# Optimization experiments

Measured on AMD Instinct MI355X. Metric: run time of the kernel, lower is better.

## Reference

```python
import jax, jax.numpy as jnp
import numpy as np

TOP_K = 2
EPS = 1e-6

def setup_inputs() -> dict:
    key = jax.random.key(0)
    ks = jax.random.split(key, 4)
    B, L, D, E, ED = 2, 2048, 2048, 8, 2048
    scale_gu = (6.0 / D) ** 0.5   # kaiming_uniform-ish bound
    scale_dn = (6.0 / ED) ** 0.5
    return {
        "x": jax.random.normal(ks[0], (B, L, D), jnp.float32),
        "router_scale": jnp.ones((D,), jnp.float32),
        "gate_w": jax.random.normal(ks[1], (D, E), jnp.float32) * (D ** -0.5),
        "gate_up": jax.random.uniform(ks[2], (E, D, 2 * ED), jnp.float32, -scale_gu, scale_gu),
        "down": jax.random.uniform(ks[3], (E, ED, D), jnp.float32, -scale_dn, scale_dn),
        "per_expert_scale": jnp.ones((E,), jnp.float32),
    }

def reference(x, router_scale, gate_w, gate_up, down, per_expert_scale):
    B, L, D = x.shape
    E = gate_up.shape[0]
    # --- Router: RMSNorm (no scale) * D^-0.5 * router_scale -> linear -> softmax -> topk -> renorm
    h = x * jax.lax.rsqrt(jnp.mean(x * x, axis=-1, keepdims=True) + EPS)
    h = h * (D ** -0.5) * router_scale
    logits = (h @ gate_w).astype(jnp.float32)            # [B,L,E]
    probs = jax.nn.softmax(logits, axis=-1)
    w, idx = jax.lax.top_k(probs, TOP_K)                 # [B,L,K]
    w = w / jnp.clip(jnp.sum(w, axis=-1, keepdims=True), 1e-12)
    w = w.astype(x.dtype)
    # --- Experts: dense compute over all experts, weighted combine by routing
    N = B * L
    xf = x.reshape(N, D)
    idxf = idx.reshape(N, TOP_K)
    wf = w.reshape(N, TOP_K)
    # combine[n,e] = sum_k wf[n,k] * (idxf[n,k]==e); top_k indices are distinct per token
    combine = jnp.zeros((N, E), x.dtype).at[jnp.arange(N)[:, None], idxf].add(wf)
    hh = jnp.einsum('nd,edf->nef', xf, gate_up)          # [N,E,2*ED]
    gate, up = jnp.split(hh, 2, axis=-1)
    act = jax.nn.gelu(gate, approximate=False) * up      # [N,E,ED]
    y = jnp.einsum('nef,efd->ned', act, down)            # [N,E,D]
    out = jnp.einsum('ne,ned->nd', combine * per_expert_scale, y)
    return out.reshape(B, L, D)
```

## Files before the change

### kernel.cpp

```cpp
#include <hip/hip_runtime.h>
#include <hip/hip_bf16.h>
#include <math.h>

#define NTOK 4096
#define DM   2048
#define NE   8
#define NKT  32

using f32x4  = float __attribute__((ext_vector_type(4)));
using bf16x8 = __bf16 __attribute__((ext_vector_type(8)));
using u32x4  = unsigned int __attribute__((ext_vector_type(4)));

#define SBAR()  __builtin_amdgcn_s_barrier()
#define SCHED() __builtin_amdgcn_sched_barrier(0)

__device__ __forceinline__ unsigned short bf16bits(float f){
  unsigned u = __builtin_bit_cast(unsigned, f);
  return (unsigned short)((u + 0x7fffu + ((u >> 16) & 1u)) >> 16);
}

__device__ __forceinline__ void load_lds16(const void* g, void* l){
  __builtin_amdgcn_global_load_lds(
      (const __attribute__((address_space(1))) unsigned int*)g,
      (__attribute__((address_space(3))) unsigned int*)l, 16, 0, 0);
}

__device__ __forceinline__ unsigned lds_addr(const void* p){
  return (unsigned)(unsigned long long)
      (__attribute__((address_space(3))) const char*)p;
}

template<int IMM>
__device__ __forceinline__ bf16x8 lds_read16(unsigned addr){
  u32x4 r;
  asm volatile("ds_read_b128 %0, %1 offset:%c2" : "=v"(r) : "v"(addr), "i"(IMM));
  return __builtin_bit_cast(bf16x8, r);
}

__global__ __launch_bounds__(256) void router_kernel(
    const float* __restrict__ x, const float* __restrict__ rs,
    const float* __restrict__ gw, const float* __restrict__ pes,
    unsigned short* __restrict__ xbf, int* __restrict__ cnt,
    int* __restrict__ toklist, float* __restrict__ slotw)
{
  const int wv = threadIdx.x >> 6, l = threadIdx.x & 63;
  const int n = blockIdx.x * 4 + wv;
  const float* xr = x + (size_t)n * DM;
  unsigned short* xb = xbf + (size_t)n * DM;
  float ssq = 0.f;
  float lg[8] = {0,0,0,0,0,0,0,0};
  #pragma unroll
  for (int q = 0; q < 8; ++q){
    int c4 = l + 64 * q;
    float4 v = ((const float4*)xr)[c4];
    float4 r = ((const float4*)rs)[c4];
    ssq += v.x*v.x + v.y*v.y + v.z*v.z + v.w*v.w;
    ushort4 o; o.x = bf16bits(v.x); o.y = bf16bits(v.y); o.z = bf16bits(v.z); o.w = bf16bits(v.w);
    ((ushort4*)xb)[c4] = o;
    float xs0 = v.x*r.x, xs1 = v.y*r.y, xs2 = v.z*r.z, xs3 = v.w*r.w;
    const float4* gp = (const float4*)(gw + (size_t)c4 * 32);
    float4 ga, gb;
    ga = gp[0]; gb = gp[1];
    lg[0]+=xs0*ga.x; lg[1]+=xs0*ga.y; lg[2]+=xs0*ga.z; lg[3]+=xs0*ga.w;
    lg[4]+=xs0*gb.x; lg[5]+=xs0*gb.y; lg[6]+=xs0*gb.z; lg[7]+=xs0*gb.w;
    ga = gp[2]; gb = gp[3];
    lg[0]+=xs1*ga.x; lg[1]+=xs1*ga.y; lg[2]+=xs1*ga.z; lg[3]+=xs1*ga.w;
    lg[4]+=xs1*gb.x; lg[5]+=xs1*gb.y; lg[6]+=xs1*gb.z; lg[7]+=xs1*gb.w;
    ga = gp[4]; gb = gp[5];
    lg[0]+=xs2*ga.x; lg[1]+=xs2*ga.y; lg[2]+=xs2*ga.z; lg[3]+=xs2*ga.w;
    lg[4]+=xs2*gb.x; lg[5]+=xs2*gb.y; lg[6]+=xs2*gb.z; lg[7]+=xs2*gb.w;
    ga = gp[6]; gb = gp[7];
    lg[0]+=xs3*ga.x; lg[1]+=xs3*ga.y; lg[2]+=xs3*ga.z; lg[3]+=xs3*ga.w;
    lg[4]+=xs3*gb.x; lg[5]+=xs3*gb.y; lg[6]+=xs3*gb.z; lg[7]+=xs3*gb.w;
  }
  #pragma unroll
  for (int off = 32; off; off >>= 1){
    ssq += __shfl_xor(ssq, off, 64);
    #pragma unroll
    for (int e2 = 0; e2 < 8; ++e2) lg[e2] += __shfl_xor(lg[e2], off, 64);
  }
  if (l == 0){
    float c = rsqrtf(ssq * (1.0f/DM) + 1e-6f) * 0.022097086912079608f;
    float mx = -1e30f;
    #pragma unroll
    for (int e2 = 0; e2 < 8; ++e2){ lg[e2] *= c; mx = fmaxf(mx, lg[e2]); }
    float l0 = lg[0]; int i0 = 0;
    #pragma unroll
    for (int e2 = 1; e2 < 8; ++e2) if (lg[e2] > l0){ l0 = lg[e2]; i0 = e2; }
    int i1 = (i0 == 0) ? 1 : 0; float l1 = (i0 == 0) ? lg[1] : lg[0];
    #pragma unroll
    for (int e2 = 0; e2 < 8; ++e2){ if (e2 != i0 && lg[e2] > l1){ l1 = lg[e2]; i1 = e2; } }
    float p0 = expf(l0 - mx), p1 = expf(l1 - mx);
    float sw = fmaxf(p0 + p1, 1e-12f);
    float w0 = p0 / sw, w1 = p1 / sw;
    int s0 = atomicAdd(&cnt[i0], 1);
    toklist[i0 * NTOK + s0] = n;
    slotw[i0 * NTOK + s0] = w0 * pes[i0];
    int s1 = atomicAdd(&cnt[i1], 1);
    toklist[i1 * NTOK + s1] = n;
    slotw[i1 * NTOK + s1] = w1 * pes[i1];
  }
}

__global__ void scan_kernel(const int* __restrict__ cnt, int* __restrict__ basep){
  if (threadIdx.x == 0){
    int a = 0;
    for (int e = 0; e < NE; ++e){ basep[e] = a; a += cnt[e]; }
  }
}

__global__ __launch_bounds__(256) void conv_transpose_kernel(
    const float* __restrict__ W, unsigned short* __restrict__ Wt, int ncols)
{
  const int z = blockIdx.z;
  const float* src = W + (size_t)z * 2048 * ncols;
  unsigned short* dst = Wt + (size_t)z * ncols * 2048;
  const int n0 = blockIdx.x * 64, k0 = blockIdx.y * 64;
  __shared__ __align__(16) unsigned short t[64][72];
  const int tid = threadIdx.x;
  const int kl = tid >> 4;
  const int nl = (tid & 15) * 4;
  #pragma unroll
  for (int q = 0; q < 4; ++q){
    int k = kl + q * 16;
    float4 v = *(const float4*)(src + (size_t)(k0 + k) * ncols + n0 + nl);
    t[nl+0][k] = bf16bits(v.x);
    t[nl+1][k] = bf16bits(v.y);
    t[nl+2][k] = bf16bits(v.z);
    t[nl+3][k] = bf16bits(v.w);
  }
  __syncthreads();
  const int nr = tid >> 3;
  const int k8 = (tid & 7) * 8;
  #pragma unroll
  for (int q = 0; q < 2; ++q){
    int n = nr + q * 32;
    u32x4 v = *(const u32x4*)&t[n][k8];
    *(u32x4*)(dst + (size_t)(n0 + n) * 2048 + k0 + k8) = v;
  }
}

template<int MODE>
__global__ __launch_bounds__(512, 2) void moe_gemm(
    const unsigned short* __restrict__ Abuf,
    const unsigned short* __restrict__ Wt,
    unsigned short* __restrict__ act,
    float* __restrict__ out,
    const int* __restrict__ cnt,
    const int* __restrict__ basep,
    const int* __restrict__ toklist,
    const float* __restrict__ slotw,
    int e0)
{
  const int z = blockIdx.z, e = e0 + z;
  const int ce = cnt[e];
  const int m0 = blockIdx.y * 256;
  if (m0 >= ce) return;
  const int fb = blockIdx.x * (MODE == 0 ? 128 : 256);
  const int tid = threadIdx.x;
  const int l = tid & 63;
  const int wv = tid >> 6;
  const int wr = wv >> 2;
  const int wc = wv & 3;
  const int baseE = basep[e];
  const size_t ncols = (MODE == 0) ? 4096 : 2048;
  const unsigned short* Wz = Wt + (size_t)z * ncols * 2048;

  __shared__ __align__(16) unsigned char smem[2][4][16384];

  const unsigned short* asrcp[2];
  const unsigned short* bsrcp[2];
  #pragma unroll
  for (int q = 0; q < 2; ++q){
    int c = q * 512 + tid;
    int rl = c >> 2;
    int gl = (c & 3) ^ ((rl >> 1) & 3);
    long rsrc;
    if (MODE == 0) rsrc = toklist[e * NTOK + min(m0 + rl, ce - 1)];
    else           rsrc = baseE + min(m0 + rl, ce - 1);
    asrcp[q] = Abuf + (size_t)rsrc * 2048 + gl * 8;
    int n;
    if (MODE == 0) n = fb + (rl >> 6) * 32 + (rl & 31) + ((rl & 32) ? 2048 : 0);
    else           n = fb + rl;
    bsrcp[q] = Wz + (size_t)n * 2048 + gl * 8;
  }
  const int dst16 = tid * 16;

  auto stage = [&](int buf, int piece, int isB, int ksrc){
    unsigned char* base = &smem[buf][piece][0];
    if (isB){
      load_lds16(bsrcp[0] + ksrc, base + dst16);
      load_lds16(bsrcp[1] + ksrc, base + 8192 + dst16);
    } else {
      load_lds16(asrcp[0] + ksrc, base + dst16);
      load_lds16(asrcp[1] + ksrc, base + 8192 + dst16);
    }
  };

  const unsigned lbase = lds_addr(&smem[0][0][0]);
  const int kq = l >> 4;
  unsigned aoffs[2][4], boffs[4];
  #pragma unroll
  for (int h = 0; h < 2; ++h)
    #pragma unroll
    for (int m = 0; m < 4; ++m){
      int row = wr * 128 + h * 64 + m * 16 + (l & 15);
      aoffs[h][m] = row * 64 + (unsigned)((kq ^ ((row >> 1) & 3)) * 16);
    }
  #pragma unroll
  for (int n = 0; n < 4; ++n){
    int col = wc * 64 + n * 16 + (l & 15);
    boffs[n] = col * 64 + (unsigned)((kq ^ ((col >> 1) & 3)) * 16);
  }

  f32x4 acc[8][4];
  #pragma unroll
  for (int i = 0; i < 8; ++i)
    #pragma unroll
    for (int j = 0; j < 4; ++j)
      acc[i][j] = (f32x4){0.f, 0.f, 0.f, 0.f};

  stage(0, 0, 0, 0);
  stage(0, 2, 1, 0);
  stage(0, 1, 0, 32);
  stage(0, 3, 1, 32);
  stage(1, 0, 0, 64);
  stage(1, 2, 1, 64);
  SCHED();
  asm volatile("s_waitcnt vmcnt(8)");
  SCHED();
  SBAR();
  SCHED();

  #pragma unroll 1
  for (int kt = 0; kt < NKT; ++kt){
    const int buf = kt & 1;
    const unsigned cb = lbase + (unsigned)buf * 65536;
    int kA1 = (kt + 1) * 64 + 32; if (kA1 > 2016) kA1 = 2016;
    int kN0 = (kt + 2) * 64;      if (kN0 > 2016) kN0 = 2016;
    bf16x8 bfr[4];

    {
      bf16x8 af[4];
      #pragma unroll
      for (int m = 0; m < 4; ++m) af[m] = lds_read16<0>(cb + aoffs[0][m]);
      #pragma unroll
      for (int n = 0; n < 4; ++n) bfr[n] = lds_read16<32768>(cb + boffs[n]);
      stage(buf ^ 1, 1, 0, kA1);
      SCHED(); SBAR();
      asm volatile("s_waitcnt lgkmcnt(0)");
      SCHED();
      __builtin_amdgcn_s_setprio(1);
      #pragma unroll
      for (int n = 0; n < 4; ++n)
        #pragma unroll
        for (int m = 0; m < 4; ++m)
          acc[m][n] = __builtin_amdgcn_mfma_f32_16x16x32_bf16(af[m], bfr[n], acc[m][n], 0, 0, 0);
      __builtin_amdgcn_s_setprio(0);
      SCHED(); SBAR(); SCHED();
    }
    {
      bf16x8 af[4];
      #pragma unroll
      for (int m = 0; m < 4; ++m) af[m] = lds_read16<0>(cb + aoffs[1][m]);
      stage(buf ^ 1, 3, 1, kA1);
      SCHED(); SBAR();
      asm volatile("s_waitcnt lgkmcnt(0)");
      SCHED();
      __builtin_amdgcn_s_setprio(1);
      #pragma unroll
      for (int n = 0; n < 4; ++n)
        #pragma unroll
        for (int m = 0; m < 4; ++m)
          acc[4 + m][n] = __builtin_amdgcn_mfma_f32_16x16x32_bf16(af[m], bfr[n], acc[4 + m][n], 0, 0, 0);
      __builtin_amdgcn_s_setprio(0);
      SCHED();
      asm volatile("s_waitcnt vmcnt(8)");
      SCHED(); SBAR(); SCHED();
    }
    {
      bf16x8 af[4];
      #pragma unroll
      for (int m = 0; m < 4; ++m) af[m] = lds_read16<16384>(cb + aoffs[0][m]);
      #pragma unroll
      for (int n = 0; n < 4; ++n) bfr[n] = lds_read16<49152>(cb + boffs[n]);
      stage(buf, 0, 0, kN0);
      SCHED(); SBAR();
      asm volatile("s_waitcnt lgkmcnt(0)");
      SCHED();
      __builtin_amdgcn_s_setprio(1);
      #pragma unroll
      for (int n = 0; n < 4; ++n)
        #pragma unroll
        for (int m = 0; m < 4; ++m)
          acc[m][n] = __builtin_amdgcn_mfma_f32_16x16x32_bf16(af[m], bfr[n], acc[m][n], 0, 0, 0);
      __builtin_amdgcn_s_setprio(0);
      SCHED(); SBAR(); SCHED();
    }
    {
      bf16x8 af[4];
      #pragma unroll
      for (int m = 0; m < 4; ++m) af[m] = lds_read16<16384>(cb + aoffs[1][m]);
      stage(buf, 2, 1, kN0);
      SCHED(); SBAR();
      asm volatile("s_waitcnt lgkmcnt(0)");
      SCHED();
      __builtin_amdgcn_s_setprio(1);
      #pragma unroll
      for (int n = 0; n < 4; ++n)
        #pragma unroll
        for (int m = 0; m < 4; ++m)
          acc[4 + m][n] = __builtin_amdgcn_mfma_f32_16x16x32_bf16(af[m], bfr[n], acc[4 + m][n], 0, 0, 0);
      __builtin_amdgcn_s_setprio(0);
      SCHED();
      asm volatile("s_waitcnt vmcnt(8)");
      SCHED(); SBAR(); SCHED();
    }
  }
  asm volatile("s_waitcnt vmcnt(0)");
  SCHED();
  SBAR();

  const int lq4 = (l >> 4) * 4;
  if (MODE == 0){
    #pragma unroll
    for (int mi = 0; mi < 8; ++mi)
      #pragma unroll
      for (int j = 0; j < 4; ++j){
        int s = m0 + wr * 128 + mi * 16 + lq4 + j;
        if (s < ce){
          size_t rowb = (size_t)(baseE + s) * 2048;
          #pragma unroll
          for (int p = 0; p < 2; ++p){
            float g = acc[mi][p][j];
            float u = acc[mi][p + 2][j];
            float a = 0.5f * g * (1.0f + erff(g * 0.70710678118654752f)) * u;
            act[rowb + fb + wc * 32 + p * 16 + (l & 15)] = bf16bits(a);
          }
        }
      }
  } else {
    #pragma unroll
    for (int mi = 0; mi < 8; ++mi)
      #pragma unroll
      for (int j = 0; j < 4; ++j){
        int s = m0 + wr * 128 + mi * 16 + lq4 + j;
        if (s < ce){
          int tokn = toklist[e * NTOK + s];
          float wgt = slotw[e * NTOK + s];
          float* orow = out + (size_t)tokn * 2048 + fb + wc * 64 + (l & 15);
          #pragma unroll
          for (int ni = 0; ni < 4; ++ni)
            atomicAdd(&orow[ni * 16], wgt * acc[mi][ni][j]);
        }
      }
  }
}

extern "C" void kernel_launch(void* const* d_in, const int* in_sizes, int n_in,
                              void* d_out, int out_size, void* d_ws, size_t ws_size,
                              hipStream_t stream)
{
  const float* x   = (const float*)d_in[0];
  const float* rs  = (const float*)d_in[1];
  const float* gw  = (const float*)d_in[2];
  const float* w1  = (const float*)d_in[3];
  const float* w2  = (const float*)d_in[4];
  const float* pes = (const float*)d_in[5];
  float* out = (float*)d_out;

  char* ws = (char*)d_ws;
  int*   cnt      = (int*)ws;
  int*   basep    = (int*)(ws + 64);
  int*   toklist  = (int*)(ws + 256);
  float* slotw    = (float*)(ws + 256 + (size_t)NE * NTOK * 4);
  unsigned short* xbf  = (unsigned short*)(ws + 256 + 2 * (size_t)NE * NTOK * 4);
  unsigned short* act  = xbf + (size_t)NTOK * DM;
  unsigned short* wtb  = act + (size_t)2 * NTOK * DM;

  const size_t fixed = (size_t)((char*)wtb - ws);
  const size_t per_e = (size_t)4096 * 2048 * 2;

  hipMemsetAsync(out, 0, (size_t)out_size * sizeof(float), stream);
  hipMemsetAsync(cnt, 0, 64, stream);
  router_kernel<<<NTOK / 4, 256, 0, stream>>>(x, rs, gw, pes, xbf, cnt, toklist, slotw);
  scan_kernel<<<1, 64, 0, stream>>>(cnt, basep);

  if (ws_size >= fixed + (size_t)NE * per_e){
    conv_transpose_kernel<<<dim3(64, 32, NE), 256, 0, stream>>>(w1, wtb, 4096);
    moe_gemm<0><<<dim3(16, 16, NE), 512, 0, stream>>>(
        xbf, wtb, act, out, cnt, basep, toklist, slotw, 0);
    conv_transpose_kernel<<<dim3(32, 32, NE), 256, 0, stream>>>(w2, wtb, 2048);
    moe_gemm<1><<<dim3(8, 16, NE), 512, 0, stream>>>(
        act, wtb, act, out, cnt, basep, toklist, slotw, 0);
  } else {
    int EG = (int)((ws_size - fixed) / per_e);
    if (EG < 1) EG = 1;
    if (EG > NE) EG = NE;
    for (int g = 0; g < NE; g += EG){
      int gg = min(EG, NE - g);
      conv_transpose_kernel<<<dim3(64, 32, gg), 256, 0, stream>>>(
          w1 + (size_t)g * 2048 * 4096, wtb, 4096);
      moe_gemm<0><<<dim3(16, 16, gg), 512, 0, stream>>>(
          xbf, wtb, act, out, cnt, basep, toklist, slotw, g);
    }
    for (int g = 0; g < NE; g += EG){
      int gg = min(EG, NE - g);
      conv_transpose_kernel<<<dim3(32, 32, gg), 256, 0, stream>>>(
          w2 + (size_t)g * 2048 * 2048, wtb, 2048);
      moe_gemm<1><<<dim3(8, 16, gg), 512, 0, stream>>>(
          act, wtb, act, out, cnt, basep, toklist, slotw, g);
    }
  }
}
```

Measured before the change: 559.6 us.

## Make MoE GEMMs persistent with compacted tile list and XCD-aware scheduling

Replaces the 3D grid, in which many blocks exit early for empty expert row-tiles, with a 256-block persistent grid. Each block walks a compacted list of (expert, m-tile, n-tile) work items built from per-expert counts. Work is split by blockIdx&7 so that all tiles of one token group land on the same XCD, aiming to reuse activation rows in that XCD's L2. The trade-off is concurrency: with 256 resident blocks at two blocks per CU, half the occupancy slots may sit idle, and the per-tile loop adds setup overhead. The low-workspace fallback now transposes all experts at once, which assumes the workspace is large enough, and a dummy shared-memory pad was added.

```diff
diff --git a/kernel.cpp b/kernel.cpp
--- a/kernel.cpp
+++ b/kernel.cpp
@@ -149,53 +149,25 @@
     const int* __restrict__ cnt,
     const int* __restrict__ basep,
     const int* __restrict__ toklist,
-    const float* __restrict__ slotw,
-    int e0)
+    const float* __restrict__ slotw)
 {
-  const int z = blockIdx.z, e = e0 + z;
-  const int ce = cnt[e];
-  const int m0 = blockIdx.y * 256;
-  if (m0 >= ce) return;
-  const int fb = blockIdx.x * (MODE == 0 ? 128 : 256);
   const int tid = threadIdx.x;
   const int l = tid & 63;
   const int wv = tid >> 6;
   const int wr = wv >> 2;
   const int wc = wv & 3;
-  const int baseE = basep[e];
+  const int w = blockIdx.x & 7;
+  const int p = blockIdx.x >> 3;
   const size_t ncols = (MODE == 0) ? 4096 : 2048;
-  const unsigned short* Wz = Wt + (size_t)z * ncols * 2048;
 
   __shared__ __align__(16) unsigned char smem[2][4][16384];
-
-  const unsigned short* asrcp[2];
-  const unsigned short* bsrcp[2];
-  #pragma unroll
-  for (int q = 0; q < 2; ++q){
-    int c = q * 512 + tid;
-    int rl = c >> 2;
-    int gl = (c & 3) ^ ((rl >> 1) & 3);
-    long rsrc;
-    if (MODE == 0) rsrc = toklist[e * NTOK + min(m0 + rl, ce - 1)];
-    else           rsrc = baseE + min(m0 + rl, ce - 1);
-    asrcp[q] = Abuf + (size_t)rsrc * 2048 + gl * 8;
-    int n;
-    if (MODE == 0) n = fb + (rl >> 6) * 32 + (rl & 31) + ((rl & 32) ? 2048 : 0);
-    else           n = fb + rl;
-    bsrcp[q] = Wz + (size_t)n * 2048 + gl * 8;
-  }
-  const int dst16 = tid * 16;
-
-  auto stage = [&](int buf, int piece, int isB, int ksrc){
-    unsigned char* base = &smem[buf][piece][0];
-    if (isB){
-      load_lds16(bsrcp[0] + ksrc, base + dst16);
-      load_lds16(bsrcp[1] + ksrc, base + 8192 + dst16);
-    } else {
-      load_lds16(asrcp[0] + ksrc, base + dst16);
-      load_lds16(asrcp[1] + ksrc, base + 8192 + dst16);
-    }
-  };
+  __shared__ unsigned char diagpad[MODE ? 544 : 16];
+  if (basep[0] == -1) *(volatile unsigned char*)&diagpad[tid & 15] = 1;
+
+  int nyv[NE], gbv[NE];
+  int G = 0;
+  #pragma unroll
+  for (int e2 = 0; e2 < NE; ++e2){ gbv[e2] = G; nyv[e2] = (cnt[e2] + 255) >> 8; G += nyv[e2]; }
 
   const unsigned lbase = lds_addr(&smem[0][0][0]);
   const int kq = l >> 4;
@@ -212,148 +184,192 @@
     int col = wc * 64 + n * 16 + (l & 15);
     boffs[n] = col * 64 + (unsigned)((kq ^ ((col >> 1) & 3)) * 16);
   }
-
-  f32x4 acc[8][4];
-  #pragma unroll
-  for (int i = 0; i < 8; ++i)
-    #pragma unroll
-    for (int j = 0; j < 4; ++j)
-      acc[i][j] = (f32x4){0.f, 0.f, 0.f, 0.f};
-
-  stage(0, 0, 0, 0);
-  stage(0, 2, 1, 0);
-  stage(0, 1, 0, 32);
-  stage(0, 3, 1, 32);
-  stage(1, 0, 0, 64);
-  stage(1, 2, 1, 64);
-  SCHED();
-  asm volatile("s_waitcnt vmcnt(8)");
-  SCHED();
-  SBAR();
-  SCHED();
+  const int dst16 = tid * 16;
+  const int lq4 = (l >> 4) * 4;
 
   #pragma unroll 1
-  for (int kt = 0; kt < NKT; ++kt){
-    const int buf = kt & 1;
-    const unsigned cb = lbase + (unsigned)buf * 65536;
-    int kA1 = (kt + 1) * 64 + 32; if (kA1 > 2016) kA1 = 2016;
-    int kN0 = (kt + 2) * 64;      if (kN0 > 2016) kN0 = 2016;
-    bf16x8 bfr[4];
-
-    {
-      bf16x8 af[4];
+  for (int idx = p; ; idx += 32){
+    int g, fbi;
+    if (MODE == 0){ fbi = idx & 15; g = w + 8 * (idx >> 4); }
+    else          { fbi = idx & 7;  g = w + 8 * (idx >> 3); }
+    if (g >= G) break;
+    int e = 0;
+    while (g >= gbv[e] + nyv[e]) ++e;
+    const int ce = cnt[e];
+    const int m0 = (g - gbv[e]) * 256;
+    const int fb = fbi * (MODE == 0 ? 128 : 256);
+    const int baseE = basep[e];
+    const unsigned short* Wz = Wt + (size_t)e * ncols * 2048;
+
+    const unsigned short* asrcp[2];
+    const unsigned short* bsrcp[2];
+    #pragma unroll
+    for (int q = 0; q < 2; ++q){
+      int c = q * 512 + tid;
+      int rl = c >> 2;
+      int gl = (c & 3) ^ ((rl >> 1) & 3);
+      long rsrc;
+      if (MODE == 0) rsrc = toklist[e * NTOK + min(m0 + rl, ce - 1)];
+      else           rsrc = baseE + min(m0 + rl, ce - 1);
+      asrcp[q] = Abuf + (size_t)rsrc * 2048 + gl * 8;
+      int n;
+      if (MODE == 0) n = fb + (rl >> 6) * 32 + (rl & 31) + ((rl & 32) ? 2048 : 0);
+      else           n = fb + rl;
+      bsrcp[q] = Wz + (size_t)n * 2048 + gl * 8;
+    }
+
+    auto stage = [&](int buf, int piece, int isB, int ksrc){
+      unsigned char* base = &smem[buf][piece][0];
+      if (isB){
+        load_lds16(bsrcp[0] + ksrc, base + dst16);
+        load_lds16(bsrcp[1] + ksrc, base + 8192 + dst16);
+      } else {
+        load_lds16(asrcp[0] + ksrc, base + dst16);
+        load_lds16(asrcp[1] + ksrc, base + 8192 + dst16);
+      }
+    };
+
+    f32x4 acc[8][4];
+    #pragma unroll
+    for (int i = 0; i < 8; ++i)
       #pragma unroll
-      for (int m = 0; m < 4; ++m) af[m] = lds_read16<0>(cb + aoffs[0][m]);
+      for (int j = 0; j < 4; ++j)
+        acc[i][j] = (f32x4){0.f, 0.f, 0.f, 0.f};
+
+    stage(0, 0, 0, 0);
+    stage(0, 2, 1, 0);
+    stage(0, 1, 0, 32);
+    stage(0, 3, 1, 32);
+    stage(1, 0, 0, 64);
+    stage(1, 2, 1, 64);
+    SCHED();
+    asm volatile("s_waitcnt vmcnt(8)");
+    SCHED();
+    SBAR();
+    SCHED();
+
+    #pragma unroll 1
+    for (int kt = 0; kt < NKT; ++kt){
+      const int buf = kt & 1;
+      const unsigned cb = lbase + (unsigned)buf * 65536;
+      int kA1 = (kt + 1) * 64 + 32; if (kA1 > 2016) kA1 = 2016;
+      int kN0 = (kt + 2) * 64;      if (kN0 > 2016) kN0 = 2016;
+      bf16x8 bfr[4];
+
+      {
+        bf16x8 af[4];
+        #pragma unroll
+        for (int m = 0; m < 4; ++m) af[m] = lds_read16<0>(cb + aoffs[0][m]);
+        #pragma unroll
+        for (int n = 0; n < 4; ++n) bfr[n] = lds_read16<32768>(cb + boffs[n]);
+        stage(buf ^ 1, 1, 0, kA1);
+        SCHED(); SBAR();
+        asm volatile("s_waitcnt lgkmcnt(0)");
+        SCHED();
+        __builtin_amdgcn_s_setprio(1);
+        #pragma unroll
+        for (int n = 0; n < 4; ++n)
+          #pragma unroll
+          for (int m = 0; m < 4; ++m)
+            acc[m][n] = __builtin_amdgcn_mfma_f32_16x16x32_bf16(af[m], bfr[n], acc[m][n], 0, 0, 0);
+        __builtin_amdgcn_s_setprio(0);
+        SCHED(); SBAR(); SCHED();
+      }
+      {
+        bf16x8 af[4];
+        #pragma unroll
+        for (int m = 0; m < 4; ++m) af[m] = lds_read16<0>(cb + aoffs[1][m]);
+        stage(buf ^ 1, 3, 1, kA1);
+        SCHED(); SBAR();
+        asm volatile("s_waitcnt lgkmcnt(0)");
+        SCHED();
+        __builtin_amdgcn_s_setprio(1);
+        #pragma unroll
+        for (int n = 0; n < 4; ++n)
+          #pragma unroll
+          for (int m = 0; m < 4; ++m)
+            acc[4 + m][n] = __builtin_amdgcn_mfma_f32_16x16x32_bf16(af[m], bfr[n], acc[4 + m][n], 0, 0, 0);
+        __builtin_amdgcn_s_setprio(0);
+        SCHED();
+        asm volatile("s_waitcnt vmcnt(8)");
+        SCHED(); SBAR(); SCHED();
+      }
+      {
+        bf16x8 af[4];
+        #pragma unroll
+        for (int m = 0; m < 4; ++m) af[m] = lds_read16<16384>(cb + aoffs[0][m]);
+        #pragma unroll
+        for (int n = 0; n < 4; ++n) bfr[n] = lds_read16<49152>(cb + boffs[n]);
+        stage(buf, 0, 0, kN0);
+        SCHED(); SBAR();
+        asm volatile("s_waitcnt lgkmcnt(0)");
+        SCHED();
+        __builtin_amdgcn_s_setprio(1);
+        #pragma unroll
+        for (int n = 0; n < 4; ++n)
+          #pragma unroll
+          for (int m = 0; m < 4; ++m)
+            acc[m][n] = __builtin_amdgcn_mfma_f32_16x16x32_bf16(af[m], bfr[n], acc[m][n], 0, 0, 0);
+        __builtin_amdgcn_s_setprio(0);
+        SCHED(); SBAR(); SCHED();
+      }
+      {
+        bf16x8 af[4];
+        #pragma unroll
+        for (int m = 0; m < 4; ++m) af[m] = lds_read16<16384>(cb + aoffs[1][m]);
+        stage(buf, 2, 1, kN0);
+        SCHED(); SBAR();
+        asm volatile("s_waitcnt lgkmcnt(0)");
+        SCHED();
+        __builtin_amdgcn_s_setprio(1);
+        #pragma unroll
+        for (int n = 0; n < 4; ++n)
+          #pragma unroll
+          for (int m = 0; m < 4; ++m)
+            acc[4 + m][n] = __builtin_amdgcn_mfma_f32_16x16x32_bf16(af[m], bfr[n], acc[4 + m][n], 0, 0, 0);
+        __builtin_amdgcn_s_setprio(0);
+        SCHED();
+        asm volatile("s_waitcnt vmcnt(8)");
+        SCHED(); SBAR(); SCHED();
+      }
+    }
+    asm volatile("s_waitcnt vmcnt(0)");
+    SCHED();
+    SBAR();
+
+    if (MODE == 0){
       #pragma unroll
-      for (int n = 0; n < 4; ++n) bfr[n] = lds_read16<32768>(cb + boffs[n]);
-      stage(buf ^ 1, 1, 0, kA1);
-      SCHED(); SBAR();
-      asm volatile("s_waitcnt lgkmcnt(0)");
-      SCHED();
-      __builtin_amdgcn_s_setprio(1);
-      #pragma unroll
-      for (int n = 0; n < 4; ++n)
-        #pragma unroll
-        for (int m = 0; m < 4; ++m)
-          acc[m][n] = __builtin_amdgcn_mfma_f32_16x16x32_bf16(af[m], bfr[n], acc[m][n], 0, 0, 0);
-      __builtin_amdgcn_s_setprio(0);
-      SCHED(); SBAR(); SCHED();
-    }
-    {
-      bf16x8 af[4];
-      #pragma unroll
-      for (int m = 0; m < 4; ++m) af[m] = lds_read16<0>(cb + aoffs[1][m]);
-      stage(buf ^ 1, 3, 1, kA1);
-      SCHED(); SBAR();
-      asm volatile("s_waitcnt lgkmcnt(0)");
-      SCHED();
-      __builtin_amdgcn_s_setprio(1);
-      #pragma unroll
-      for (int n = 0; n < 4; ++n)
-        #pragma unroll
-        for (int m = 0; m < 4; ++m)
-          acc[4 + m][n] = __builtin_amdgcn_mfma_f32_16x16x32_bf16(af[m], bfr[n], acc[4 + m][n], 0, 0, 0);
-      __builtin_amdgcn_s_setprio(0);
-      SCHED();
-      asm volatile("s_waitcnt vmcnt(8)");
-      SCHED(); SBAR(); SCHED();
-    }
-    {
-      bf16x8 af[4];
-      #pragma unroll
-      for (int m = 0; m < 4; ++m) af[m] = lds_read16<16384>(cb + aoffs[0][m]);
-      #pragma unroll
-      for (int n = 0; n < 4; ++n) bfr[n] = lds_read16<49152>(cb + boffs[n]);
-      stage(buf, 0, 0, kN0);
-      SCHED(); SBAR();
-      asm volatile("s_waitcnt lgkmcnt(0)");
-      SCHED();
-      __builtin_amdgcn_s_setprio(1);
-      #pragma unroll
-      for (int n = 0; n < 4; ++n)
-        #pragma unroll
-        for (int m = 0; m < 4; ++m)
-          acc[m][n] = __builtin_amdgcn_mfma_f32_16x16x32_bf16(af[m], bfr[n], acc[m][n], 0, 0, 0);
-      __builtin_amdgcn_s_setprio(0);
-      SCHED(); SBAR(); SCHED();
-    }
-    {
-      bf16x8 af[4];
-      #pragma unroll
-      for (int m = 0; m < 4; ++m) af[m] = lds_read16<16384>(cb + aoffs[1][m]);
-      stage(buf, 2, 1, kN0);
-      SCHED(); SBAR();
-      asm volatile("s_waitcnt lgkmcnt(0)");
-      SCHED();
-      __builtin_amdgcn_s_setprio(1);
-      #pragma unroll
-      for (int n = 0; n < 4; ++n)
-        #pragma unroll
-        for (int m = 0; m < 4; ++m)
-          acc[4 + m][n] = __builtin_amdgcn_mfma_f32_16x16x32_bf16(af[m], bfr[n], acc[4 + m][n], 0, 0, 0);
-      __builtin_amdgcn_s_setprio(0);
-      SCHED();
-      asm volatile("s_waitcnt vmcnt(8)");
-      SCHED(); SBAR(); SCHED();
-    }
-  }
-  asm volatile("s_waitcnt vmcnt(0)");
-  SCHED();
-  SBAR();
-
-  const int lq4 = (l >> 4) * 4;
-  if (MODE == 0){
-    #pragma unroll
-    for (int mi = 0; mi < 8; ++mi)
-      #pragma unroll
-      for (int j = 0; j < 4; ++j){
-        int s = m0 + wr * 128 + mi * 16 + lq4 + j;
-        if (s < ce){
-          size_t rowb = (size_t)(baseE + s) * 2048;
-          #pragma unroll
-          for (int p = 0; p < 2; ++p){
-            float g = acc[mi][p][j];
-            float u = acc[mi][p + 2][j];
-            float a = 0.5f * g * (1.0f + erff(g * 0.70710678118654752f)) * u;
-            act[rowb + fb + wc * 32 + p * 16 + (l & 15)] = bf16bits(a);
+      for (int mi = 0; mi < 8; ++mi)
+        #pragma unroll
+        for (int j = 0; j < 4; ++j){
+          int s = m0 + wr * 128 + mi * 16 + lq4 + j;
+          if (s < ce){
+            size_t rowb = (size_t)(baseE + s) * 2048;
+            #pragma unroll
+            for (int pq = 0; pq < 2; ++pq){
+              float gg = acc[mi][pq][j];
+              float uu = acc[mi][pq + 2][j];
+              float a = 0.5f * gg * (1.0f + erff(gg * 0.70710678118654752f)) * uu;
+              act[rowb + fb + wc * 32 + pq * 16 + (l & 15)] = bf16bits(a);
+            }
           }
         }
-      }
-  } else {
-    #pragma unroll
-    for (int mi = 0; mi < 8; ++mi)
+    } else {
       #pragma unroll
-      for (int j = 0; j < 4; ++j){
-        int s = m0 + wr * 128 + mi * 16 + lq4 + j;
-        if (s < ce){
-          int tokn = toklist[e * NTOK + s];
-          float wgt = slotw[e * NTOK + s];
-          float* orow = out + (size_t)tokn * 2048 + fb + wc * 64 + (l & 15);
-          #pragma unroll
-          for (int ni = 0; ni < 4; ++ni)
-            atomicAdd(&orow[ni * 16], wgt * acc[mi][ni][j]);
+      for (int mi = 0; mi < 8; ++mi)
+        #pragma unroll
+        for (int j = 0; j < 4; ++j){
+          int s = m0 + wr * 128 + mi * 16 + lq4 + j;
+          if (s < ce){
+            int tokn = toklist[e * NTOK + s];
+            float wgt = slotw[e * NTOK + s];
+            float* orow = out + (size_t)tokn * 2048 + fb + wc * 64 + (l & 15);
+            #pragma unroll
+            for (int ni = 0; ni < 4; ++ni)
+              atomicAdd(&orow[ni * 16], wgt * acc[mi][ni][j]);
+          }
         }
-      }
+    }
   }
 }
 
@@ -388,28 +404,17 @@
 
   if (ws_size >= fixed + (size_t)NE * per_e){
     conv_transpose_kernel<<<dim3(64, 32, NE), 256, 0, stream>>>(w1, wtb, 4096);
-    moe_gemm<0><<<dim3(16, 16, NE), 512, 0, stream>>>(
-        xbf, wtb, act, out, cnt, basep, toklist, slotw, 0);
+    moe_gemm<0><<<256, 512, 0, stream>>>(xbf, wtb, act, out, cnt, basep, toklist, slotw);
     conv_transpose_kernel<<<dim3(32, 32, NE), 256, 0, stream>>>(w2, wtb, 2048);
-    moe_gemm<1><<<dim3(8, 16, NE), 512, 0, stream>>>(
-        act, wtb, act, out, cnt, basep, toklist, slotw, 0);
+    moe_gemm<1><<<256, 512, 0, stream>>>(act, wtb, act, out, cnt, basep, toklist, slotw);
   } else {
-    int EG = (int)((ws_size - fixed) / per_e);
-    if (EG < 1) EG = 1;
-    if (EG > NE) EG = NE;
-    for (int g = 0; g < NE; g += EG){
-      int gg = min(EG, NE - g);
-      conv_transpose_kernel<<<dim3(64, 32, gg), 256, 0, stream>>>(
-          w1 + (size_t)g * 2048 * 4096, wtb, 4096);
-      moe_gemm<0><<<dim3(16, 16, gg), 512, 0, stream>>>(
-          xbf, wtb, act, out, cnt, basep, toklist, slotw, g);
-    }
-    for (int g = 0; g < NE; g += EG){
-      int gg = min(EG, NE - g);
-      conv_transpose_kernel<<<dim3(32, 32, gg), 256, 0, stream>>>(
-          w2 + (size_t)g * 2048 * 2048, wtb, 2048);
-      moe_gemm<1><<<dim3(8, 16, gg), 512, 0, stream>>>(
-          act, wtb, act, out, cnt, basep, toklist, slotw, g);
-    }
-  }
-}
+    int half = NE / 2;
+    size_t w1half = (size_t)half * 2048 * 4096;
+    conv_transpose_kernel<<<dim3(64, 32, half), 256, 0, stream>>>(w1, wtb, 4096);
+    conv_transpose_kernel<<<dim3(64, 32, half), 256, 0, stream>>>(
+        w1 + w1half, wtb + (size_t)half * 4096 * 2048, 4096);
+    moe_gemm<0><<<256, 512, 0, stream>>>(xbf, wtb, act, out, cnt, basep, toklist, slotw);
+    conv_transpose_kernel<<<dim3(32, 32, NE), 256, 0, stream>>>(w2, wtb, 2048);
+    moe_gemm<1><<<256, 512, 0, stream>>>(act, wtb, act, out, cnt, basep, toklist, slotw);
+  }
+}
```

Result: slower. 584.9 us (+4.5%).

## Software-pipeline LDS fragment reads against MFMA clusters with double-buffered registers

Applied to the files above, without the earlier changes.

Restructures the GEMM main loop so the LDS fragment reads for the next quarter-step are issued before the current MFMA cluster runs. A and B fragments are held in ping-pong register sets, which cuts one barrier per phase and hides LDS latency behind matrix math. A small extra shared-memory pad is added behind a never-taken store; it changes the LDS footprint, apparently to shift occupancy or bank mapping. The cost is more vector registers, with a risk of spills at 2 blocks per CU, and a more delicate barrier and waitcnt ordering.

```diff
diff --git a/kernel.cpp b/kernel.cpp
--- a/kernel.cpp
+++ b/kernel.cpp
@@ -139,6 +139,16 @@
     *(u32x4*)(dst + (size_t)(n0 + n) * 2048 + k0 + k8) = v;
   }
 }
+
+#define MFMA_CLUSTER(AF, BF, BASE)                                              \
+  __builtin_amdgcn_s_setprio(1);                                                \
+  _Pragma("unroll")                                                             \
+  for (int n_ = 0; n_ < 4; ++n_)                                                \
+    _Pragma("unroll")                                                           \
+    for (int m_ = 0; m_ < 4; ++m_)                                              \
+      acc[BASE + m_][n_] = __builtin_amdgcn_mfma_f32_16x16x32_bf16(             \
+          AF[m_], BF[n_], acc[BASE + m_][n_], 0, 0, 0);                         \
+  __builtin_amdgcn_s_setprio(0);
 
 template<int MODE>
 __global__ __launch_bounds__(512, 2) void moe_gemm(
@@ -167,6 +177,8 @@
   const unsigned short* Wz = Wt + (size_t)z * ncols * 2048;
 
   __shared__ __align__(16) unsigned char smem[2][4][16384];
+  __shared__ unsigned char diagpad[MODE ? 544 : 16];
+  if (basep[0] == -1) *(volatile unsigned char*)&diagpad[tid & 15] = 1;
 
   const unsigned short* asrcp[2];
   const unsigned short* bsrcp[2];
@@ -220,6 +232,8 @@
     for (int j = 0; j < 4; ++j)
       acc[i][j] = (f32x4){0.f, 0.f, 0.f, 0.f};
 
+  bf16x8 afA[4], afB[4], bfrA[4], bfrB[4];
+
   stage(0, 0, 0, 0);
   stage(0, 2, 1, 0);
   stage(0, 1, 0, 32);
@@ -231,93 +245,64 @@
   SCHED();
   SBAR();
   SCHED();
+  #pragma unroll
+  for (int m = 0; m < 4; ++m) afA[m] = lds_read16<0>(lbase + aoffs[0][m]);
+  #pragma unroll
+  for (int n = 0; n < 4; ++n) bfrA[n] = lds_read16<32768>(lbase + boffs[n]);
+  SCHED();
 
   #pragma unroll 1
   for (int kt = 0; kt < NKT; ++kt){
-    const int buf = kt & 1;
-    const unsigned cb = lbase + (unsigned)buf * 65536;
+    const unsigned cb = lbase + (unsigned)(kt & 1) * 65536;
+    const unsigned nb = lbase + (unsigned)((kt & 1) ^ 1) * 65536;
     int kA1 = (kt + 1) * 64 + 32; if (kA1 > 2016) kA1 = 2016;
     int kN0 = (kt + 2) * 64;      if (kN0 > 2016) kN0 = 2016;
-    bf16x8 bfr[4];
-
-    {
-      bf16x8 af[4];
-      #pragma unroll
-      for (int m = 0; m < 4; ++m) af[m] = lds_read16<0>(cb + aoffs[0][m]);
-      #pragma unroll
-      for (int n = 0; n < 4; ++n) bfr[n] = lds_read16<32768>(cb + boffs[n]);
-      stage(buf ^ 1, 1, 0, kA1);
-      SCHED(); SBAR();
-      asm volatile("s_waitcnt lgkmcnt(0)");
-      SCHED();
-      __builtin_amdgcn_s_setprio(1);
-      #pragma unroll
-      for (int n = 0; n < 4; ++n)
-        #pragma unroll
-        for (int m = 0; m < 4; ++m)
-          acc[m][n] = __builtin_amdgcn_mfma_f32_16x16x32_bf16(af[m], bfr[n], acc[m][n], 0, 0, 0);
-      __builtin_amdgcn_s_setprio(0);
-      SCHED(); SBAR(); SCHED();
-    }
-    {
-      bf16x8 af[4];
-      #pragma unroll
-      for (int m = 0; m < 4; ++m) af[m] = lds_read16<0>(cb + aoffs[1][m]);
-      stage(buf ^ 1, 3, 1, kA1);
-      SCHED(); SBAR();
-      asm volatile("s_waitcnt lgkmcnt(0)");
-      SCHED();
-      __builtin_amdgcn_s_setprio(1);
-      #pragma unroll
-      for (int n = 0; n < 4; ++n)
-        #pragma unroll
-        for (int m = 0; m < 4; ++m)
-          acc[4 + m][n] = __builtin_amdgcn_mfma_f32_16x16x32_bf16(af[m], bfr[n], acc[4 + m][n], 0, 0, 0);
-      __builtin_amdgcn_s_setprio(0);
-      SCHED();
-      asm volatile("s_waitcnt vmcnt(8)");
-      SCHED(); SBAR(); SCHED();
-    }
-    {
-      bf16x8 af[4];
-      #pragma unroll
-      for (int m = 0; m < 4; ++m) af[m] = lds_read16<16384>(cb + aoffs[0][m]);
-      #pragma unroll
-      for (int n = 0; n < 4; ++n) bfr[n] = lds_read16<49152>(cb + boffs[n]);
-      stage(buf, 0, 0, kN0);
-      SCHED(); SBAR();
-      asm volatile("s_waitcnt lgkmcnt(0)");
-      SCHED();
-      __builtin_amdgcn_s_setprio(1);
-      #pragma unroll
-      for (int n = 0; n < 4; ++n)
-        #pragma unroll
-        for (int m = 0; m < 4; ++m)
-          acc[m][n] = __builtin_amdgcn_mfma_f32_16x16x32_bf16(af[m], bfr[n], acc[m][n], 0, 0, 0);
-      __builtin_amdgcn_s_setprio(0);
-      SCHED(); SBAR(); SCHED();
-    }
-    {
-      bf16x8 af[4];
-      #pragma unroll
-      for (int m = 0; m < 4; ++m) af[m] = lds_read16<16384>(cb + aoffs[1][m]);
-      stage(buf, 2, 1, kN0);
-      SCHED(); SBAR();
-      asm volatile("s_waitcnt lgkmcnt(0)");
-      SCHED();
-      __builtin_amdgcn_s_setprio(1);
-      #pragma unroll
-      for (int n = 0; n < 4; ++n)
-        #pragma unroll
-        for (int m = 0; m < 4; ++m)
-          acc[4 + m][n] = __builtin_amdgcn_mfma_f32_16x16x32_bf16(af[m], bfr[n], acc[4 + m][n], 0, 0, 0);
-      __builtin_amdgcn_s_setprio(0);
-      SCHED();
-      asm volatile("s_waitcnt vmcnt(8)");
-      SCHED(); SBAR(); SCHED();
-    }
-  }
-  asm volatile("s_waitcnt vmcnt(0)");
+
+    stage((kt & 1) ^ 1, 1, 0, kA1);
+    asm volatile("s_waitcnt lgkmcnt(0)");
+    SCHED();
+    #pragma unroll
+    for (int m = 0; m < 4; ++m) afB[m] = lds_read16<0>(cb + aoffs[1][m]);
+    SCHED();
+    MFMA_CLUSTER(afA, bfrA, 0)
+    SCHED(); SBAR(); SCHED();
+
+    stage((kt & 1) ^ 1, 3, 1, kA1);
+    asm volatile("s_waitcnt lgkmcnt(0)");
+    SCHED();
+    asm volatile("s_waitcnt vmcnt(8)");
+    SCHED();
+    #pragma unroll
+    for (int m = 0; m < 4; ++m) afA[m] = lds_read16<16384>(cb + aoffs[0][m]);
+    #pragma unroll
+    for (int n = 0; n < 4; ++n) bfrB[n] = lds_read16<49152>(cb + boffs[n]);
+    SCHED();
+    MFMA_CLUSTER(afB, bfrA, 4)
+    SCHED(); SBAR(); SCHED();
+
+    stage(kt & 1, 0, 0, kN0);
+    asm volatile("s_waitcnt lgkmcnt(0)");
+    SCHED();
+    #pragma unroll
+    for (int m = 0; m < 4; ++m) afB[m] = lds_read16<16384>(cb + aoffs[1][m]);
+    SCHED();
+    MFMA_CLUSTER(afA, bfrB, 0)
+    SCHED(); SBAR(); SCHED();
+
+    stage(kt & 1, 2, 1, kN0);
+    asm volatile("s_waitcnt lgkmcnt(0)");
+    SCHED();
+    asm volatile("s_waitcnt vmcnt(8)");
+    SCHED();
+    #pragma unroll
+    for (int m = 0; m < 4; ++m) afA[m] = lds_read16<0>(nb + aoffs[0][m]);
+    #pragma unroll
+    for (int n = 0; n < 4; ++n) bfrA[n] = lds_read16<32768>(nb + boffs[n]);
+    SCHED();
+    MFMA_CLUSTER(afB, bfrB, 4)
+    SCHED(); SBAR(); SCHED();
+  }
+  asm volatile("s_waitcnt vmcnt(0) lgkmcnt(0)");
   SCHED();
   SBAR();
 
```

Measured after the change: 548.0 us. 1.02x faster.
